# Performance work log

Measured on AMD Instinct MI355X. Metric: run time of the kernel, lower is better.

The kernel has to match this reference:

```python
import jax, jax.numpy as jnp
import numpy as np

CLUSTER_DIM = 64
SHRINKAGE = True
EPS = 1e-8


def setup_inputs() -> dict:
    key = jax.random.key(0)
    x = jax.random.normal(key, (256, CLUSTER_DIM, 4096), dtype=jnp.float32)
    return {"x": x}


def _mat_shrinkage(C, n):
    # Rao-Blackwellized Ledoit-Wolf shrinkage toward scaled identity.
    p = CLUSTER_DIM
    I = jnp.eye(p, dtype=C.dtype)[None, :, :]
    trace = jnp.trace(C, axis1=-2, axis2=-1)[:, None, None]          # [B,1,1]
    F_hat = trace / p * I
    second_trace = jnp.einsum('bij,bji->b', C, C)[:, None, None]      # tr(C @ C)
    numerator = (n - 2) / n * second_trace + trace ** 2
    denominator = (n + 2) * (second_trace - trace ** 2 / p)
    rho = jnp.minimum(numerator / denominator, 1.0)
    return rho * F_hat + (1.0 - rho) * C


def reference(x):
    B, C, M = x.shape  # C == CLUSTER_DIM
    x_mu = jnp.mean(x, axis=2, keepdims=True)
    x_cnt = x - x_mu                                                  # [B,C,M]
    cov = jnp.einsum('bcm,bdm->bcd', x_cnt, x_cnt) / M                # [B,C,C]
    if SHRINKAGE:
        cov = _mat_shrinkage(cov, n=M)
    L, Q = jnp.linalg.eigh(cov)                                       # L:[B,C] Q:[B,C,C]
    L = jnp.maximum(L, EPS)
    # S_hat = Q @ diag(L^-1/2) @ Q^T, fused as scaled columns of Q
    S_hat = jnp.einsum('bik,bk,bjk->bij', Q, jax.lax.rsqrt(L), Q)     # [B,C,C]
    Z = jnp.einsum('bij,bjm->bim', S_hat, x_cnt)                      # [B,C,M]
    return Z
```

## Files before the change

### kernel.cpp

```cpp
#include <hip/hip_runtime.h>
#include <hip/hip_bf16.h>

#define BB 256
#define P 64
#define MM 4096
#define MC 128
#define MT 256

using bf16x8 = __attribute__((ext_vector_type(8))) short;
using f32x16 = __attribute__((ext_vector_type(16))) float;
using f32x4  = __attribute__((ext_vector_type(4))) float;

__device__ inline f32x16 MF(bf16x8 a, bf16x8 b, f32x16 c) {
    return __builtin_amdgcn_mfma_f32_32x32x16_bf16(a, b, c, 0, 0, 0);
}
__device__ inline unsigned cvtpk(float lo, float hi) {
    unsigned u;
    asm("v_cvt_pk_bf16_f32 %0, %1, %2" : "=v"(u) : "v"(lo), "v"(hi));
    return u;
}

__global__ __launch_bounds__(256)
void covpart_kernel(const float* __restrict__ x, float* __restrict__ s2p,
                    float* __restrict__ s1p, int nsplit)
{
    __shared__ __align__(16) unsigned char smem[34816];

    const int b = blockIdx.x, sp = blockIdx.y;
    const int t = threadIdx.x;
    const int w = t >> 6, l = t & 63;
    const int lr = l & 31, lh = l >> 5;
    const int mlen = MM / nsplit;
    const float* xb = x + (size_t)b * (P * MM) + (size_t)sp * mlen;

    f32x16 acc0 = {0,0,0,0,0,0,0,0,0,0,0,0,0,0,0,0};
    f32x16 acc1 = {0,0,0,0,0,0,0,0,0,0,0,0,0,0,0,0};
    f32x16 acc2 = {0,0,0,0,0,0,0,0,0,0,0,0,0,0,0,0};
    float s1a[8] = {0.f,0.f,0.f,0.f,0.f,0.f,0.f,0.f};

    const int kbase = lh * 16;
    const int nch = mlen / MC;

    f32x4 v[8];
    #pragma unroll
    for (int j = 0; j < 8; ++j) {
        int f4 = t + 256 * j;
        int r = f4 >> 5, c = (f4 & 31) << 2;
        v[j] = *reinterpret_cast<const f32x4*>(xb + (size_t)r * MM + c);
    }

    for (int ch = 0; ch < nch; ++ch) {
        char* buf = (char*)smem + (ch & 1) * 17408;
        #pragma unroll
        for (int j = 0; j < 8; ++j) {
            int f4 = t + 256 * j;
            int r = f4 >> 5, c4 = f4 & 31;
            float e0 = v[j].x, e1 = v[j].y, e2 = v[j].z, e3 = v[j].w;
            s1a[j] += (e0 + e1) + (e2 + e3);
            uint2 hp;
            hp.x = cvtpk(e0, e1);
            hp.y = cvtpk(e2, e3);
            *reinterpret_cast<uint2*>(buf + r * 272 + c4 * 8) = hp;
        }
        if (ch + 1 < nch) {
            const int m0 = (ch + 1) * MC;
            #pragma unroll
            for (int j = 0; j < 8; ++j) {
                int f4 = t + 256 * j;
                int r = f4 >> 5, c = (f4 & 31) << 2;
                v[j] = *reinterpret_cast<const f32x4*>(xb + (size_t)r * MM + m0 + c);
            }
        }
        __syncthreads();
        #pragma unroll
        for (int kk = 0; kk < 2; ++kk) {
            const int kb = (2 * w + kk) * 32 + kbase;
            bf16x8 f0 = *(const bf16x8*)(buf + lr * 272 + kb);
            bf16x8 f1 = *(const bf16x8*)(buf + (32 + lr) * 272 + kb);
            acc0 = MF(f0, f0, acc0);
            acc1 = MF(f0, f1, acc1);
            acc2 = MF(f1, f1, acc2);
        }
    }

    float (*T)[32][33] = reinterpret_cast<float (*)[32][33]>(smem);
    float* s2b = s2p + ((size_t)sp * BB + b) * (P * P);

#define REDUCE_PASS(ACC, STORE)                                       \
    {                                                                 \
        __syncthreads();                                              \
        _Pragma("unroll")                                             \
        for (int n = 0; n < 16; ++n) {                                \
            int row = (n & 3) + 8 * (n >> 2) + 4 * lh;                \
            T[w][row][lr] = ACC[n];                                   \
        }                                                             \
        __syncthreads();                                              \
        _Pragma("unroll")                                             \
        for (int q = 0; q < 4; ++q) {                                 \
            int idx = t + 256 * q;                                    \
            int r = idx >> 5, c = idx & 31;                           \
            float s = T[0][r][c] + T[1][r][c] + T[2][r][c] + T[3][r][c]; \
            STORE                                                     \
        }                                                             \
    }

    REDUCE_PASS(acc0, s2b[r * 64 + c] = s;)
    REDUCE_PASS(acc1, s2b[r * 64 + 32 + c] = s; s2b[(32 + c) * 64 + r] = s;)
    REDUCE_PASS(acc2, s2b[(32 + r) * 64 + 32 + c] = s;)
#undef REDUCE_PASS

    #pragma unroll
    for (int m = 16; m >= 1; m >>= 1) {
        #pragma unroll
        for (int j = 0; j < 8; ++j) s1a[j] += __shfl_xor(s1a[j], m);
    }
    if ((l & 31) == 0) {
        float* s1b = s1p + ((size_t)sp * BB + b) * P;
        int r0 = 2 * w + lh;
        #pragma unroll
        for (int j = 0; j < 8; ++j) s1b[r0 + 8 * j] = s1a[j];
    }
}

typedef float (*Mat68)[68];

__device__ inline void mm64f(Mat68 D, Mat68 A, Mat68 Bm, int t, float alpha, float beta)
{
    __syncthreads();
    const int r0 = (t >> 4) * 4, c0 = (t & 15) * 4;
    float acc[4][4];
    #pragma unroll
    for (int i = 0; i < 4; ++i)
        #pragma unroll
        for (int j = 0; j < 4; ++j) acc[i][j] = 0.f;
    #pragma unroll 4
    for (int k = 0; k < P; ++k) {
        float av[4], bv[4];
        *reinterpret_cast<float4*>(av) = *reinterpret_cast<const float4*>(&A[k][r0]);
        *reinterpret_cast<float4*>(bv) = *reinterpret_cast<const float4*>(&Bm[k][c0]);
        #pragma unroll
        for (int i = 0; i < 4; ++i)
            #pragma unroll
            for (int j = 0; j < 4; ++j) acc[i][j] += av[i] * bv[j];
    }
    __syncthreads();
    #pragma unroll
    for (int i = 0; i < 4; ++i)
        #pragma unroll
        for (int j = 0; j < 4; ++j)
            D[r0 + i][c0 + j] = alpha * acc[i][j] + ((r0 + i) == (c0 + j) ? beta : 0.f);
}

__global__ __launch_bounds__(256)
void whiten_kernel(const float* __restrict__ s2p, const float* __restrict__ s1p,
                   unsigned* __restrict__ sbb, float* __restrict__ tvec, int nsplit)
{
    __shared__ __align__(16) float B0[P][68], B1[P][68], B2[P][68], B3[P][68], B4[P][68];
    __shared__ float mus[P];
    __shared__ float red[2][4];
    const int b = blockIdx.x, t = threadIdx.x;

    if (t < P) {
        float s = 0.f;
        for (int sp = 0; sp < nsplit; ++sp) s += s1p[((size_t)sp * BB + b) * P + t];
        mus[t] = s * (1.0f / MM);
    }
    __syncthreads();

    float tr_part = 0.f, s2_part = 0.f;
    #pragma unroll
    for (int j = 0; j < 16; ++j) {
        int f = t + 256 * j;
        int i = f >> 6, jc = f & 63;
        float sum = 0.f;
        for (int sp = 0; sp < nsplit; ++sp)
            sum += s2p[((size_t)sp * BB + b) * (P * P) + f];
        float v = sum * (1.0f / MM) - mus[i] * mus[jc];
        B0[i][jc] = v;
        s2_part += v * v;
        if (i == jc) tr_part += v;
    }
    #pragma unroll
    for (int off = 32; off > 0; off >>= 1) {
        tr_part += __shfl_down(tr_part, off);
        s2_part += __shfl_down(s2_part, off);
    }
    if ((t & 63) == 0) { red[0][t >> 6] = tr_part; red[1][t >> 6] = s2_part; }
    __syncthreads();
    const float trace = red[0][0] + red[0][1] + red[0][2] + red[0][3];
    const float sum2  = red[1][0] + red[1][1] + red[1][2] + red[1][3];

    const float nf = (float)MM;
    const float num = (nf - 2.0f) / nf * sum2 + trace * trace;
    const float den = (nf + 2.0f) * (sum2 - trace * trace / (float)P);
    const float rho = (den > 0.f) ? fminf(num / den, 1.0f) : 1.0f;
    const float lam = trace * (1.0f / P);
    const float inv_s = 1.0f / lam;

    #pragma unroll
    for (int j = 0; j < 16; ++j) {
        int f = t + 256 * j;
        int i = f >> 6, jc = f & 63;
        float v = B0[i][jc];
        float sv = ((1.0f - rho) * v + ((i == jc) ? rho * lam : 0.f)) * inv_s;
        B0[i][jc] = sv;
        B2[i][jc] = ((i == jc) ? 1.5f : 0.f) - 0.5f * sv;
    }

    mm64f(B1, B0, B2, t, 1.f, 0.f);
    Mat68 Yc = B1, Zc = B2, Tc = B0, U = B3, V = B4;
    {
        mm64f(Tc, Zc, Yc, t, -0.5f, 1.5f);
        mm64f(U,  Yc, Tc, t, 1.f, 0.f);
        mm64f(V,  Tc, Zc, t, 1.f, 0.f);
        Mat68 tmp = Yc; Yc = U; U = tmp;
        tmp = Zc; Zc = V; V = tmp;
    }
    mm64f(Tc, Zc, Yc, t, -0.5f, 1.5f);
    mm64f(U,  Tc, Zc, t, 1.f, 0.f);
    __syncthreads();

    const float sc = rsqrtf(lam);
    unsigned* sb = sbb + (size_t)b * (P * P / 2);
    #pragma unroll
    for (int j = 0; j < 8; ++j) {
        int slot = t + 256 * j;
        int dp = slot >> 6, row = slot & 63;
        sb[slot] = cvtpk(U[row][2 * dp] * sc, U[row][2 * dp + 1] * sc);
    }
    if (t < P) {
        float tv = 0.f;
        #pragma unroll
        for (int d = 0; d < P; ++d) tv += U[t][d] * mus[d];
        tvec[b * P + t] = tv * sc;
    }
}

__global__ __launch_bounds__(256)
void apply_kernel(const float* __restrict__ x, const unsigned* __restrict__ sbb,
                  const float* __restrict__ tvec, float* __restrict__ out)
{
    __shared__ unsigned Spk[32][68];
    __shared__ unsigned Xpk[32][260];
    __shared__ float tvs[P];
    const int mt = blockIdx.x, b = blockIdx.y;
    const int t = threadIdx.x;
    const int w = t >> 6, l = t & 63;
    const int lr = l & 31, lh = l >> 5;

    const unsigned* sb = sbb + (size_t)b * (P * P / 2);
    #pragma unroll
    for (int j = 0; j < 8; ++j) {
        int slot = t + 256 * j;
        Spk[slot >> 6][slot & 63] = sb[slot];
    }
    if (t < P) tvs[t] = tvec[b * P + t];

    const float* xb = x + (size_t)b * (P * MM) + mt * MT;
    #pragma unroll
    for (int j = 0; j < 8; ++j) {
        int slot = t + 256 * j;
        int dp = slot >> 6, m0 = (slot & 63) * 4;
        const float* xr = xb + (size_t)(2 * dp) * MM + m0;
        f32x4 a = __builtin_nontemporal_load(reinterpret_cast<const f32x4*>(xr));
        f32x4 c = __builtin_nontemporal_load(reinterpret_cast<const f32x4*>(xr + MM));
        uint4 pk = make_uint4(cvtpk(a.x, c.x), cvtpk(a.y, c.y),
                              cvtpk(a.z, c.z), cvtpk(a.w, c.w));
        *reinterpret_cast<uint4*>(&Xpk[dp][m0]) = pk;
    }
    __syncthreads();

    union U8 { unsigned u[4]; bf16x8 v; };
    bf16x8 sa0[4], sa1[4];
    #pragma unroll
    for (int ks = 0; ks < 4; ++ks) {
        const int dpb = ks * 8 + lh * 4;
        U8 x0, x1;
        #pragma unroll
        for (int q = 0; q < 4; ++q) {
            x0.u[q] = Spk[dpb + q][lr];
            x1.u[q] = Spk[dpb + q][32 + lr];
        }
        sa0[ks] = x0.v;
        sa1[ks] = x1.v;
    }

    f32x16 acc00 = {0,0,0,0,0,0,0,0,0,0,0,0,0,0,0,0};
    f32x16 acc01 = {0,0,0,0,0,0,0,0,0,0,0,0,0,0,0,0};
    f32x16 acc10 = {0,0,0,0,0,0,0,0,0,0,0,0,0,0,0,0};
    f32x16 acc11 = {0,0,0,0,0,0,0,0,0,0,0,0,0,0,0,0};

    const int cq0 = (2 * w) * 32 + lr, cq1 = cq0 + 32;
    #pragma unroll
    for (int ks = 0; ks < 4; ++ks) {
        const int dpb = ks * 8 + lh * 4;
        U8 b0, b1;
        #pragma unroll
        for (int q = 0; q < 4; ++q) {
            b0.u[q] = Xpk[dpb + q][cq0];
            b1.u[q] = Xpk[dpb + q][cq1];
        }
        acc00 = MF(sa0[ks], b0.v, acc00);
        acc01 = MF(sa0[ks], b1.v, acc01);
        acc10 = MF(sa1[ks], b0.v, acc10);
        acc11 = MF(sa1[ks], b1.v, acc11);
    }

    float* ob = out + (size_t)b * (P * MM) + mt * MT;
#define STORE_TILE(ACC, RT, CQ)                                          \
    {                                                                    \
        _Pragma("unroll")                                                \
        for (int n = 0; n < 16; ++n) {                                   \
            int row = (RT) * 32 + (n & 3) + 8 * (n >> 2) + 4 * lh;       \
            __builtin_nontemporal_store(ACC[n] - tvs[row],               \
                                        ob + (size_t)row * MM + (CQ));   \
        }                                                                \
    }
    STORE_TILE(acc00, 0, cq0)
    STORE_TILE(acc01, 0, cq1)
    STORE_TILE(acc10, 1, cq0)
    STORE_TILE(acc11, 1, cq1)
#undef STORE_TILE
}

extern "C" void kernel_launch(void* const* d_in, const int* in_sizes, int n_in,
                              void* d_out, int out_size, void* d_ws, size_t ws_size,
                              hipStream_t stream)
{
    const float* x = (const float*)d_in[0];
    float* out = (float*)d_out;

    auto need = [](int ns) -> size_t {
        return ((size_t)ns * BB * P * P + (size_t)ns * BB * P
                + (size_t)BB * P * P / 2 + (size_t)BB * P) * sizeof(float);
    };
    int nsplit = 4;
    if (ws_size < need(4)) nsplit = 2;
    if (ws_size < need(2)) nsplit = 1;

    float* s2p  = (float*)d_ws;
    float* s1p  = s2p + (size_t)nsplit * BB * P * P;
    unsigned* sbb = (unsigned*)(s1p + (size_t)nsplit * BB * P);
    float* tvec = (float*)(sbb + (size_t)BB * P * P / 2);

    covpart_kernel<<<dim3(BB, nsplit), 256, 0, stream>>>(x, s2p, s1p, nsplit);
    whiten_kernel<<<dim3(BB), 256, 0, stream>>>(s2p, s1p, sbb, tvec, nsplit);
    apply_kernel<<<dim3(MM / MT, BB), 256, 0, stream>>>(x, sbb, tvec, out);
}
```

Measured before the change: 196.2 us.

## Write packed bf16 copy of x in covariance pass and read it in apply

While computing covariance partials, the first kernel now also writes a row-pair-packed bf16 copy of x to workspace. The apply kernel reads that half-size buffer instead of re-reading fp32 x and converting it. This is meant to cut the apply kernel's read traffic. The price is an extra 64 MB of workspace writes in the first pass, and the path turns on only when the workspace is large enough. The fallback apply kernel also drops its nontemporal loads.

```diff
diff --git a/kernel.cpp b/kernel.cpp
--- a/kernel.cpp
+++ b/kernel.cpp
@@ -10,6 +10,8 @@
 using bf16x8 = __attribute__((ext_vector_type(8))) short;
 using f32x16 = __attribute__((ext_vector_type(16))) float;
 using f32x4  = __attribute__((ext_vector_type(4))) float;
+using u32x4  = __attribute__((ext_vector_type(4))) unsigned;
+using u32x2  = __attribute__((ext_vector_type(2))) unsigned;
 
 __device__ inline f32x16 MF(bf16x8 a, bf16x8 b, f32x16 c) {
     return __builtin_amdgcn_mfma_f32_32x32x16_bf16(a, b, c, 0, 0, 0);
@@ -20,9 +22,10 @@
     return u;
 }
 
+template<bool XPK>
 __global__ __launch_bounds__(256)
 void covpart_kernel(const float* __restrict__ x, float* __restrict__ s2p,
-                    float* __restrict__ s1p, int nsplit)
+                    float* __restrict__ s1p, unsigned* __restrict__ xpk, int nsplit)
 {
     __shared__ __align__(16) unsigned char smem[34816];
 
@@ -32,43 +35,59 @@
     const int lr = l & 31, lh = l >> 5;
     const int mlen = MM / nsplit;
     const float* xb = x + (size_t)b * (P * MM) + (size_t)sp * mlen;
+    unsigned* xpb = XPK ? (xpk + (size_t)b * (32 * MM) + (size_t)sp * mlen) : nullptr;
 
     f32x16 acc0 = {0,0,0,0,0,0,0,0,0,0,0,0,0,0,0,0};
     f32x16 acc1 = {0,0,0,0,0,0,0,0,0,0,0,0,0,0,0,0};
     f32x16 acc2 = {0,0,0,0,0,0,0,0,0,0,0,0,0,0,0,0};
-    float s1a[8] = {0.f,0.f,0.f,0.f,0.f,0.f,0.f,0.f};
+    float s1e[4] = {0.f,0.f,0.f,0.f};
+    float s1o[4] = {0.f,0.f,0.f,0.f};
 
     const int kbase = lh * 16;
     const int nch = mlen / MC;
 
-    f32x4 v[8];
-    #pragma unroll
-    for (int j = 0; j < 8; ++j) {
-        int f4 = t + 256 * j;
-        int r = f4 >> 5, c = (f4 & 31) << 2;
-        v[j] = *reinterpret_cast<const f32x4*>(xb + (size_t)r * MM + c);
+    f32x4 ve[4], vo[4];
+    #pragma unroll
+    for (int j = 0; j < 4; ++j) {
+        int slot = t + 256 * j;
+        int dp = slot >> 5, c = (slot & 31) << 2;
+        const float* p = xb + (size_t)(2 * dp) * MM + c;
+        ve[j] = *reinterpret_cast<const f32x4*>(p);
+        vo[j] = *reinterpret_cast<const f32x4*>(p + MM);
     }
 
     for (int ch = 0; ch < nch; ++ch) {
         char* buf = (char*)smem + (ch & 1) * 17408;
         #pragma unroll
-        for (int j = 0; j < 8; ++j) {
-            int f4 = t + 256 * j;
-            int r = f4 >> 5, c4 = f4 & 31;
-            float e0 = v[j].x, e1 = v[j].y, e2 = v[j].z, e3 = v[j].w;
-            s1a[j] += (e0 + e1) + (e2 + e3);
-            uint2 hp;
-            hp.x = cvtpk(e0, e1);
-            hp.y = cvtpk(e2, e3);
-            *reinterpret_cast<uint2*>(buf + r * 272 + c4 * 8) = hp;
+        for (int j = 0; j < 4; ++j) {
+            int slot = t + 256 * j;
+            int dp = slot >> 5, c4 = slot & 31;
+            float e0 = ve[j].x, e1 = ve[j].y, e2 = ve[j].z, e3 = ve[j].w;
+            float o0 = vo[j].x, o1 = vo[j].y, o2 = vo[j].z, o3 = vo[j].w;
+            s1e[j] += (e0 + e1) + (e2 + e3);
+            s1o[j] += (o0 + o1) + (o2 + o3);
+            u32x2 he, ho;
+            he.x = cvtpk(e0, e1); he.y = cvtpk(e2, e3);
+            ho.x = cvtpk(o0, o1); ho.y = cvtpk(o2, o3);
+            char* dst = buf + (2 * dp) * 272 + c4 * 8;
+            *reinterpret_cast<u32x2*>(dst) = he;
+            *reinterpret_cast<u32x2*>(dst + 272) = ho;
+            if (XPK) {
+                u32x4 pd;
+                pd.x = cvtpk(e0, o0); pd.y = cvtpk(e1, o1);
+                pd.z = cvtpk(e2, o2); pd.w = cvtpk(e3, o3);
+                *reinterpret_cast<u32x4*>(xpb + (size_t)dp * MM + ch * MC + c4 * 4) = pd;
+            }
         }
         if (ch + 1 < nch) {
             const int m0 = (ch + 1) * MC;
             #pragma unroll
-            for (int j = 0; j < 8; ++j) {
-                int f4 = t + 256 * j;
-                int r = f4 >> 5, c = (f4 & 31) << 2;
-                v[j] = *reinterpret_cast<const f32x4*>(xb + (size_t)r * MM + m0 + c);
+            for (int j = 0; j < 4; ++j) {
+                int slot = t + 256 * j;
+                int dp = slot >> 5, c = (slot & 31) << 2;
+                const float* p = xb + (size_t)(2 * dp) * MM + m0 + c;
+                ve[j] = *reinterpret_cast<const f32x4*>(p);
+                vo[j] = *reinterpret_cast<const f32x4*>(p + MM);
             }
         }
         __syncthreads();
@@ -112,13 +131,20 @@
     #pragma unroll
     for (int m = 16; m >= 1; m >>= 1) {
         #pragma unroll
-        for (int j = 0; j < 8; ++j) s1a[j] += __shfl_xor(s1a[j], m);
-    }
-    if ((l & 31) == 0) {
+        for (int j = 0; j < 4; ++j) {
+            s1e[j] += __shfl_xor(s1e[j], m);
+            s1o[j] += __shfl_xor(s1o[j], m);
+        }
+    }
+    if ((t & 31) == 0) {
         float* s1b = s1p + ((size_t)sp * BB + b) * P;
-        int r0 = 2 * w + lh;
-        #pragma unroll
-        for (int j = 0; j < 8; ++j) s1b[r0 + 8 * j] = s1a[j];
+        int g = t >> 5;
+        #pragma unroll
+        for (int j = 0; j < 4; ++j) {
+            int r0 = 2 * (g + 8 * j);
+            s1b[r0]     = s1e[j];
+            s1b[r0 + 1] = s1o[j];
+        }
     }
 }
 
@@ -237,8 +263,8 @@
 }
 
 __global__ __launch_bounds__(256)
-void apply_kernel(const float* __restrict__ x, const unsigned* __restrict__ sbb,
-                  const float* __restrict__ tvec, float* __restrict__ out)
+void apply_kernel_x(const unsigned* __restrict__ xpk, const unsigned* __restrict__ sbb,
+                    const float* __restrict__ tvec, float* __restrict__ out)
 {
     __shared__ unsigned Spk[32][68];
     __shared__ unsigned Xpk[32][260];
@@ -256,17 +282,13 @@
     }
     if (t < P) tvs[t] = tvec[b * P + t];
 
-    const float* xb = x + (size_t)b * (P * MM) + mt * MT;
+    const unsigned* xb = xpk + (size_t)b * (32 * MM) + mt * MT;
     #pragma unroll
     for (int j = 0; j < 8; ++j) {
         int slot = t + 256 * j;
         int dp = slot >> 6, m0 = (slot & 63) * 4;
-        const float* xr = xb + (size_t)(2 * dp) * MM + m0;
-        f32x4 a = __builtin_nontemporal_load(reinterpret_cast<const f32x4*>(xr));
-        f32x4 c = __builtin_nontemporal_load(reinterpret_cast<const f32x4*>(xr + MM));
-        uint4 pk = make_uint4(cvtpk(a.x, c.x), cvtpk(a.y, c.y),
-                              cvtpk(a.z, c.z), cvtpk(a.w, c.w));
-        *reinterpret_cast<uint4*>(&Xpk[dp][m0]) = pk;
+        u32x4 pk = *reinterpret_cast<const u32x4*>(xb + (size_t)dp * MM + m0);
+        *reinterpret_cast<u32x4*>(&Xpk[dp][m0]) = pk;
     }
     __syncthreads();
 
@@ -323,6 +345,93 @@
 #undef STORE_TILE
 }
 
+__global__ __launch_bounds__(256)
+void apply_kernel(const float* __restrict__ x, const unsigned* __restrict__ sbb,
+                  const float* __restrict__ tvec, float* __restrict__ out)
+{
+    __shared__ unsigned Spk[32][68];
+    __shared__ unsigned Xpk[32][260];
+    __shared__ float tvs[P];
+    const int mt = blockIdx.x, b = blockIdx.y;
+    const int t = threadIdx.x;
+    const int w = t >> 6, l = t & 63;
+    const int lr = l & 31, lh = l >> 5;
+
+    const unsigned* sb = sbb + (size_t)b * (P * P / 2);
+    #pragma unroll
+    for (int j = 0; j < 8; ++j) {
+        int slot = t + 256 * j;
+        Spk[slot >> 6][slot & 63] = sb[slot];
+    }
+    if (t < P) tvs[t] = tvec[b * P + t];
+
+    const float* xb = x + (size_t)b * (P * MM) + mt * MT;
+    #pragma unroll
+    for (int j = 0; j < 8; ++j) {
+        int slot = t + 256 * j;
+        int dp = slot >> 6, m0 = (slot & 63) * 4;
+        const float* xr = xb + (size_t)(2 * dp) * MM + m0;
+        f32x4 a = *reinterpret_cast<const f32x4*>(xr);
+        f32x4 c = *reinterpret_cast<const f32x4*>(xr + MM);
+        uint4 pk = make_uint4(cvtpk(a.x, c.x), cvtpk(a.y, c.y),
+                              cvtpk(a.z, c.z), cvtpk(a.w, c.w));
+        *reinterpret_cast<uint4*>(&Xpk[dp][m0]) = pk;
+    }
+    __syncthreads();
+
+    union U8 { unsigned u[4]; bf16x8 v; };
+    bf16x8 sa0[4], sa1[4];
+    #pragma unroll
+    for (int ks = 0; ks < 4; ++ks) {
+        const int dpb = ks * 8 + lh * 4;
+        U8 x0, x1;
+        #pragma unroll
+        for (int q = 0; q < 4; ++q) {
+            x0.u[q] = Spk[dpb + q][lr];
+            x1.u[q] = Spk[dpb + q][32 + lr];
+        }
+        sa0[ks] = x0.v;
+        sa1[ks] = x1.v;
+    }
+
+    f32x16 acc00 = {0,0,0,0,0,0,0,0,0,0,0,0,0,0,0,0};
+    f32x16 acc01 = {0,0,0,0,0,0,0,0,0,0,0,0,0,0,0,0};
+    f32x16 acc10 = {0,0,0,0,0,0,0,0,0,0,0,0,0,0,0,0};
+    f32x16 acc11 = {0,0,0,0,0,0,0,0,0,0,0,0,0,0,0,0};
+
+    const int cq0 = (2 * w) * 32 + lr, cq1 = cq0 + 32;
+    #pragma unroll
+    for (int ks = 0; ks < 4; ++ks) {
+        const int dpb = ks * 8 + lh * 4;
+        U8 b0, b1;
+        #pragma unroll
+        for (int q = 0; q < 4; ++q) {
+            b0.u[q] = Xpk[dpb + q][cq0];
+            b1.u[q] = Xpk[dpb + q][cq1];
+        }
+        acc00 = MF(sa0[ks], b0.v, acc00);
+        acc01 = MF(sa0[ks], b1.v, acc01);
+        acc10 = MF(sa1[ks], b0.v, acc10);
+        acc11 = MF(sa1[ks], b1.v, acc11);
+    }
+
+    float* ob = out + (size_t)b * (P * MM) + mt * MT;
+#define STORE_TILE(ACC, RT, CQ)                                          \
+    {                                                                    \
+        _Pragma("unroll")                                                \
+        for (int n = 0; n < 16; ++n) {                                   \
+            int row = (RT) * 32 + (n & 3) + 8 * (n >> 2) + 4 * lh;       \
+            __builtin_nontemporal_store(ACC[n] - tvs[row],               \
+                                        ob + (size_t)row * MM + (CQ));   \
+        }                                                                \
+    }
+    STORE_TILE(acc00, 0, cq0)
+    STORE_TILE(acc01, 0, cq1)
+    STORE_TILE(acc10, 1, cq0)
+    STORE_TILE(acc11, 1, cq1)
+#undef STORE_TILE
+}
+
 extern "C" void kernel_launch(void* const* d_in, const int* in_sizes, int n_in,
                               void* d_out, int out_size, void* d_ws, size_t ws_size,
                               hipStream_t stream)
@@ -334,16 +443,30 @@
         return ((size_t)ns * BB * P * P + (size_t)ns * BB * P
                 + (size_t)BB * P * P / 2 + (size_t)BB * P) * sizeof(float);
     };
-    int nsplit = 4;
-    if (ws_size < need(4)) nsplit = 2;
-    if (ws_size < need(2)) nsplit = 1;
+    const size_t xpk_bytes = (size_t)BB * 32 * MM * sizeof(unsigned);
+
+    int nsplit;
+    bool xon;
+    if (ws_size >= need(4) + xpk_bytes)      { nsplit = 4; xon = true; }
+    else if (ws_size >= need(2) + xpk_bytes) { nsplit = 2; xon = true; }
+    else {
+        xon = false;
+        nsplit = (ws_size >= need(4)) ? 4 : (ws_size >= need(2)) ? 2 : 1;
+    }
 
     float* s2p  = (float*)d_ws;
     float* s1p  = s2p + (size_t)nsplit * BB * P * P;
     unsigned* sbb = (unsigned*)(s1p + (size_t)nsplit * BB * P);
     float* tvec = (float*)(sbb + (size_t)BB * P * P / 2);
-
-    covpart_kernel<<<dim3(BB, nsplit), 256, 0, stream>>>(x, s2p, s1p, nsplit);
-    whiten_kernel<<<dim3(BB), 256, 0, stream>>>(s2p, s1p, sbb, tvec, nsplit);
-    apply_kernel<<<dim3(MM / MT, BB), 256, 0, stream>>>(x, sbb, tvec, out);
-}
+    unsigned* xpk = (unsigned*)(tvec + (size_t)BB * P);
+
+    if (xon) {
+        covpart_kernel<true><<<dim3(BB, nsplit), 256, 0, stream>>>(x, s2p, s1p, xpk, nsplit);
+        whiten_kernel<<<dim3(BB), 256, 0, stream>>>(s2p, s1p, sbb, tvec, nsplit);
+        apply_kernel_x<<<dim3(MM / MT, BB), 256, 0, stream>>>(xpk, sbb, tvec, out);
+    } else {
+        covpart_kernel<false><<<dim3(BB, nsplit), 256, 0, stream>>>(x, s2p, s1p, nullptr, nsplit);
+        whiten_kernel<<<dim3(BB), 256, 0, stream>>>(s2p, s1p, sbb, tvec, nsplit);
+        apply_kernel<<<dim3(MM / MT, BB), 256, 0, stream>>>(x, sbb, tvec, out);
+    }
+}
```

After: 187.0 us. 1.05x faster.

## Fuse covariance and whitening kernels and stage packed bf16 x for apply

Applied to the files above, without the earlier changes.

Merges the split covariance kernel and the whitening kernel into one 1024-thread block per batch. Each block accumulates the full covariance with MFMA, builds the centered covariance in LDS, and runs the Newton-Schulz iterations on 256 of its threads. This drops the partial-sum workspace round trip and one launch. The same kernel also writes a bf16 pair-packed copy of x, so the apply kernel reads half the bytes instead of re-reading fp32 x and converting it. The cost is a large extra write and a large new workspace buffer with no size check. It also uses fewer, larger blocks with a serial whitening tail during which most threads sit idle.

```diff
diff --git a/kernel.cpp b/kernel.cpp
--- a/kernel.cpp
+++ b/kernel.cpp
@@ -4,12 +4,15 @@
 #define BB 256
 #define P 64
 #define MM 4096
-#define MC 128
+#define MC2 512
+#define RS 1040
 #define MT 256
 
 using bf16x8 = __attribute__((ext_vector_type(8))) short;
 using f32x16 = __attribute__((ext_vector_type(16))) float;
 using f32x4  = __attribute__((ext_vector_type(4))) float;
+using u32x4  = __attribute__((ext_vector_type(4))) unsigned;
+using u32x2  = __attribute__((ext_vector_type(2))) unsigned;
 
 __device__ inline f32x16 MF(bf16x8 a, bf16x8 b, f32x16 c) {
     return __builtin_amdgcn_mfma_f32_32x32x16_bf16(a, b, c, 0, 0, 0);
@@ -20,73 +23,145 @@
     return u;
 }
 
-__global__ __launch_bounds__(256)
-void covpart_kernel(const float* __restrict__ x, float* __restrict__ s2p,
-                    float* __restrict__ s1p, int nsplit)
+typedef float (*M68)[68];
+
+__device__ inline void mmg(M68 D, M68 A, M68 Bm, int t, float alpha, float beta)
 {
-    __shared__ __align__(16) unsigned char smem[34816];
-
-    const int b = blockIdx.x, sp = blockIdx.y;
+    __syncthreads();
+    float acc[4][4];
+    const int r0 = (t >> 4) * 4, c0 = (t & 15) * 4;
+    if (t < 256) {
+        #pragma unroll
+        for (int i = 0; i < 4; ++i)
+            #pragma unroll
+            for (int j = 0; j < 4; ++j) acc[i][j] = 0.f;
+        #pragma unroll 4
+        for (int k = 0; k < P; ++k) {
+            float av[4], bv[4];
+            *reinterpret_cast<float4*>(av) = *reinterpret_cast<const float4*>(&A[k][r0]);
+            *reinterpret_cast<float4*>(bv) = *reinterpret_cast<const float4*>(&Bm[k][c0]);
+            #pragma unroll
+            for (int i = 0; i < 4; ++i)
+                #pragma unroll
+                for (int j = 0; j < 4; ++j) acc[i][j] += av[i] * bv[j];
+        }
+    }
+    __syncthreads();
+    if (t < 256) {
+        #pragma unroll
+        for (int i = 0; i < 4; ++i)
+            #pragma unroll
+            for (int j = 0; j < 4; ++j)
+                D[r0 + i][c0 + j] = alpha * acc[i][j] + ((r0 + i) == (c0 + j) ? beta : 0.f);
+    }
+}
+
+__global__ __launch_bounds__(1024)
+void covwhiten_kernel(const float* __restrict__ x, unsigned* __restrict__ xpk,
+                      unsigned* __restrict__ sbb, float* __restrict__ tvec)
+{
+    __shared__ __align__(16) unsigned char smem[133120];
+    __shared__ float mus[P];
+    __shared__ float red[2][16];
+    __shared__ float s1red[16][4][2];
+
+    const int b = blockIdx.x;
     const int t = threadIdx.x;
     const int w = t >> 6, l = t & 63;
     const int lr = l & 31, lh = l >> 5;
-    const int mlen = MM / nsplit;
-    const float* xb = x + (size_t)b * (P * MM) + (size_t)sp * mlen;
+    const float* xb = x + (size_t)b * (P * MM);
+    unsigned* xpb = xpk + (size_t)b * (32 * MM);
 
     f32x16 acc0 = {0,0,0,0,0,0,0,0,0,0,0,0,0,0,0,0};
     f32x16 acc1 = {0,0,0,0,0,0,0,0,0,0,0,0,0,0,0,0};
     f32x16 acc2 = {0,0,0,0,0,0,0,0,0,0,0,0,0,0,0,0};
-    float s1a[8] = {0.f,0.f,0.f,0.f,0.f,0.f,0.f,0.f};
-
+    float s1e[4] = {0.f,0.f,0.f,0.f};
+    float s1o[4] = {0.f,0.f,0.f,0.f};
     const int kbase = lh * 16;
-    const int nch = mlen / MC;
-
-    f32x4 v[8];
-    #pragma unroll
-    for (int j = 0; j < 8; ++j) {
-        int f4 = t + 256 * j;
-        int r = f4 >> 5, c = (f4 & 31) << 2;
-        v[j] = *reinterpret_cast<const f32x4*>(xb + (size_t)r * MM + c);
-    }
-
-    for (int ch = 0; ch < nch; ++ch) {
-        char* buf = (char*)smem + (ch & 1) * 17408;
-        #pragma unroll
-        for (int j = 0; j < 8; ++j) {
-            int f4 = t + 256 * j;
-            int r = f4 >> 5, c4 = f4 & 31;
-            float e0 = v[j].x, e1 = v[j].y, e2 = v[j].z, e3 = v[j].w;
-            s1a[j] += (e0 + e1) + (e2 + e3);
-            uint2 hp;
-            hp.x = cvtpk(e0, e1);
-            hp.y = cvtpk(e2, e3);
-            *reinterpret_cast<uint2*>(buf + r * 272 + c4 * 8) = hp;
-        }
-        if (ch + 1 < nch) {
-            const int m0 = (ch + 1) * MC;
+
+    f32x4 ve[4], vo[4];
+    #pragma unroll
+    for (int j = 0; j < 4; ++j) {
+        int slot = t + 1024 * j;
+        int dp = slot >> 7, c = (slot & 127) << 2;
+        const float* p = xb + (size_t)(2 * dp) * MM + c;
+        ve[j] = *reinterpret_cast<const f32x4*>(p);
+        vo[j] = *reinterpret_cast<const f32x4*>(p + MM);
+    }
+
+    for (int ch = 0; ch < MM / MC2; ++ch) {
+        char* buf = (char*)smem + (ch & 1) * 66560;
+        #pragma unroll
+        for (int j = 0; j < 4; ++j) {
+            int slot = t + 1024 * j;
+            int dp = slot >> 7, c4 = slot & 127;
+            float e0 = ve[j].x, e1 = ve[j].y, e2 = ve[j].z, e3 = ve[j].w;
+            float o0 = vo[j].x, o1 = vo[j].y, o2 = vo[j].z, o3 = vo[j].w;
+            s1e[j] += (e0 + e1) + (e2 + e3);
+            s1o[j] += (o0 + o1) + (o2 + o3);
+            u32x2 he, ho;
+            he.x = cvtpk(e0, e1); he.y = cvtpk(e2, e3);
+            ho.x = cvtpk(o0, o1); ho.y = cvtpk(o2, o3);
+            char* dst = buf + (2 * dp) * RS + c4 * 8;
+            *reinterpret_cast<u32x2*>(dst) = he;
+            *reinterpret_cast<u32x2*>(dst + RS) = ho;
+            u32x4 pd;
+            pd.x = cvtpk(e0, o0); pd.y = cvtpk(e1, o1);
+            pd.z = cvtpk(e2, o2); pd.w = cvtpk(e3, o3);
+            *reinterpret_cast<u32x4*>(xpb + (size_t)dp * MM + ch * MC2 + c4 * 4) = pd;
+        }
+        if (ch + 1 < MM / MC2) {
+            const int m0 = (ch + 1) * MC2;
             #pragma unroll
-            for (int j = 0; j < 8; ++j) {
-                int f4 = t + 256 * j;
-                int r = f4 >> 5, c = (f4 & 31) << 2;
-                v[j] = *reinterpret_cast<const f32x4*>(xb + (size_t)r * MM + m0 + c);
+            for (int j = 0; j < 4; ++j) {
+                int slot = t + 1024 * j;
+                int dp = slot >> 7, c = (slot & 127) << 2;
+                const float* p = xb + (size_t)(2 * dp) * MM + m0 + c;
+                ve[j] = *reinterpret_cast<const f32x4*>(p);
+                vo[j] = *reinterpret_cast<const f32x4*>(p + MM);
             }
         }
         __syncthreads();
         #pragma unroll
         for (int kk = 0; kk < 2; ++kk) {
             const int kb = (2 * w + kk) * 32 + kbase;
-            bf16x8 f0 = *(const bf16x8*)(buf + lr * 272 + kb);
-            bf16x8 f1 = *(const bf16x8*)(buf + (32 + lr) * 272 + kb);
+            bf16x8 f0 = *(const bf16x8*)(buf + lr * RS + kb);
+            bf16x8 f1 = *(const bf16x8*)(buf + (32 + lr) * RS + kb);
             acc0 = MF(f0, f0, acc0);
             acc1 = MF(f0, f1, acc1);
             acc2 = MF(f1, f1, acc2);
         }
     }
 
+    #pragma unroll
+    for (int m = 32; m >= 1; m >>= 1) {
+        #pragma unroll
+        for (int j = 0; j < 4; ++j) {
+            s1e[j] += __shfl_xor(s1e[j], m);
+            s1o[j] += __shfl_xor(s1o[j], m);
+        }
+    }
+    if (l == 0) {
+        #pragma unroll
+        for (int j = 0; j < 4; ++j) {
+            s1red[w][j][0] = s1e[j];
+            s1red[w][j][1] = s1o[j];
+        }
+    }
+    __syncthreads();
+    if (t < P) {
+        int par = t & 1, dh = t >> 1;
+        int d0 = dh & 7, jj = dh >> 3;
+        mus[t] = (s1red[2 * d0][jj][par] + s1red[2 * d0 + 1][jj][par]) * (1.0f / MM);
+    }
+
     float (*T)[32][33] = reinterpret_cast<float (*)[32][33]>(smem);
-    float* s2b = s2p + ((size_t)sp * BB + b) * (P * P);
-
-#define REDUCE_PASS(ACC, STORE)                                       \
+    M68 CM = reinterpret_cast<M68>((char*)smem + 69632);
+    const float invM = 1.0f / MM;
+    const int rr = t >> 5, cc = t & 31;
+    float trp = 0.f, s2p = 0.f;
+
+#define CREDUCE(ACC, BODY)                                            \
     {                                                                 \
         __syncthreads();                                              \
         _Pragma("unroll")                                             \
@@ -95,100 +170,38 @@
             T[w][row][lr] = ACC[n];                                   \
         }                                                             \
         __syncthreads();                                              \
-        _Pragma("unroll")                                             \
-        for (int q = 0; q < 4; ++q) {                                 \
-            int idx = t + 256 * q;                                    \
-            int r = idx >> 5, c = idx & 31;                           \
-            float s = T[0][r][c] + T[1][r][c] + T[2][r][c] + T[3][r][c]; \
-            STORE                                                     \
+        {                                                             \
+            float s = 0.f;                                            \
+            _Pragma("unroll")                                         \
+            for (int wv = 0; wv < 16; ++wv) s += T[wv][rr][cc];       \
+            BODY                                                      \
         }                                                             \
     }
 
-    REDUCE_PASS(acc0, s2b[r * 64 + c] = s;)
-    REDUCE_PASS(acc1, s2b[r * 64 + 32 + c] = s; s2b[(32 + c) * 64 + r] = s;)
-    REDUCE_PASS(acc2, s2b[(32 + r) * 64 + 32 + c] = s;)
-#undef REDUCE_PASS
-
-    #pragma unroll
-    for (int m = 16; m >= 1; m >>= 1) {
-        #pragma unroll
-        for (int j = 0; j < 8; ++j) s1a[j] += __shfl_xor(s1a[j], m);
-    }
-    if ((l & 31) == 0) {
-        float* s1b = s1p + ((size_t)sp * BB + b) * P;
-        int r0 = 2 * w + lh;
-        #pragma unroll
-        for (int j = 0; j < 8; ++j) s1b[r0 + 8 * j] = s1a[j];
-    }
-}
-
-typedef float (*Mat68)[68];
-
-__device__ inline void mm64f(Mat68 D, Mat68 A, Mat68 Bm, int t, float alpha, float beta)
-{
-    __syncthreads();
-    const int r0 = (t >> 4) * 4, c0 = (t & 15) * 4;
-    float acc[4][4];
-    #pragma unroll
-    for (int i = 0; i < 4; ++i)
-        #pragma unroll
-        for (int j = 0; j < 4; ++j) acc[i][j] = 0.f;
-    #pragma unroll 4
-    for (int k = 0; k < P; ++k) {
-        float av[4], bv[4];
-        *reinterpret_cast<float4*>(av) = *reinterpret_cast<const float4*>(&A[k][r0]);
-        *reinterpret_cast<float4*>(bv) = *reinterpret_cast<const float4*>(&Bm[k][c0]);
-        #pragma unroll
-        for (int i = 0; i < 4; ++i)
-            #pragma unroll
-            for (int j = 0; j < 4; ++j) acc[i][j] += av[i] * bv[j];
-    }
-    __syncthreads();
-    #pragma unroll
-    for (int i = 0; i < 4; ++i)
-        #pragma unroll
-        for (int j = 0; j < 4; ++j)
-            D[r0 + i][c0 + j] = alpha * acc[i][j] + ((r0 + i) == (c0 + j) ? beta : 0.f);
-}
-
-__global__ __launch_bounds__(256)
-void whiten_kernel(const float* __restrict__ s2p, const float* __restrict__ s1p,
-                   unsigned* __restrict__ sbb, float* __restrict__ tvec, int nsplit)
-{
-    __shared__ __align__(16) float B0[P][68], B1[P][68], B2[P][68], B3[P][68], B4[P][68];
-    __shared__ float mus[P];
-    __shared__ float red[2][4];
-    const int b = blockIdx.x, t = threadIdx.x;
-
-    if (t < P) {
-        float s = 0.f;
-        for (int sp = 0; sp < nsplit; ++sp) s += s1p[((size_t)sp * BB + b) * P + t];
-        mus[t] = s * (1.0f / MM);
-    }
-    __syncthreads();
-
-    float tr_part = 0.f, s2_part = 0.f;
-    #pragma unroll
-    for (int j = 0; j < 16; ++j) {
-        int f = t + 256 * j;
-        int i = f >> 6, jc = f & 63;
-        float sum = 0.f;
-        for (int sp = 0; sp < nsplit; ++sp)
-            sum += s2p[((size_t)sp * BB + b) * (P * P) + f];
-        float v = sum * (1.0f / MM) - mus[i] * mus[jc];
-        B0[i][jc] = v;
-        s2_part += v * v;
-        if (i == jc) tr_part += v;
-    }
-    #pragma unroll
-    for (int off = 32; off > 0; off >>= 1) {
-        tr_part += __shfl_down(tr_part, off);
-        s2_part += __shfl_down(s2_part, off);
-    }
-    if ((t & 63) == 0) { red[0][t >> 6] = tr_part; red[1][t >> 6] = s2_part; }
-    __syncthreads();
-    const float trace = red[0][0] + red[0][1] + red[0][2] + red[0][3];
-    const float sum2  = red[1][0] + red[1][1] + red[1][2] + red[1][3];
+    CREDUCE(acc0, {
+        float v = s * invM - mus[rr] * mus[cc];
+        CM[rr][cc] = v; s2p += v * v; if (rr == cc) trp += v;
+    })
+    CREDUCE(acc1, {
+        float v = s * invM - mus[rr] * mus[32 + cc];
+        CM[rr][32 + cc] = v; CM[32 + cc][rr] = v; s2p += 2.f * v * v;
+    })
+    CREDUCE(acc2, {
+        float v = s * invM - mus[32 + rr] * mus[32 + cc];
+        CM[32 + rr][32 + cc] = v; s2p += v * v; if (rr == cc) trp += v;
+    })
+#undef CREDUCE
+
+    #pragma unroll
+    for (int m = 32; m >= 1; m >>= 1) {
+        trp += __shfl_xor(trp, m);
+        s2p += __shfl_xor(s2p, m);
+    }
+    if (l == 0) { red[0][w] = trp; red[1][w] = s2p; }
+    __syncthreads();
+    float trace = 0.f, sum2 = 0.f;
+    #pragma unroll
+    for (int wv = 0; wv < 16; ++wv) { trace += red[0][wv]; sum2 += red[1][wv]; }
 
     const float nf = (float)MM;
     const float num = (nf - 2.0f) / nf * sum2 + trace * trace;
@@ -197,48 +210,46 @@
     const float lam = trace * (1.0f / P);
     const float inv_s = 1.0f / lam;
 
-    #pragma unroll
-    for (int j = 0; j < 16; ++j) {
-        int f = t + 256 * j;
+    M68 M1 = reinterpret_cast<M68>(smem);
+    M68 M2 = reinterpret_cast<M68>((char*)smem + 17408);
+    M68 M3 = reinterpret_cast<M68>((char*)smem + 34816);
+    #pragma unroll
+    for (int jj = 0; jj < 4; ++jj) {
+        int f = t + 1024 * jj;
         int i = f >> 6, jc = f & 63;
-        float v = B0[i][jc];
+        float v = CM[i][jc];
         float sv = ((1.0f - rho) * v + ((i == jc) ? rho * lam : 0.f)) * inv_s;
-        B0[i][jc] = sv;
-        B2[i][jc] = ((i == jc) ? 1.5f : 0.f) - 0.5f * sv;
-    }
-
-    mm64f(B1, B0, B2, t, 1.f, 0.f);
-    Mat68 Yc = B1, Zc = B2, Tc = B0, U = B3, V = B4;
-    {
-        mm64f(Tc, Zc, Yc, t, -0.5f, 1.5f);
-        mm64f(U,  Yc, Tc, t, 1.f, 0.f);
-        mm64f(V,  Tc, Zc, t, 1.f, 0.f);
-        Mat68 tmp = Yc; Yc = U; U = tmp;
-        tmp = Zc; Zc = V; V = tmp;
-    }
-    mm64f(Tc, Zc, Yc, t, -0.5f, 1.5f);
-    mm64f(U,  Tc, Zc, t, 1.f, 0.f);
+        CM[i][jc] = sv;
+        M2[i][jc] = ((i == jc) ? 1.5f : 0.f) - 0.5f * sv;
+    }
+
+    mmg(M1, CM, M2, t, 1.f, 0.f);
+    mmg(CM, M2, M1, t, -0.5f, 1.5f);
+    mmg(M3, M1, CM, t, 1.f, 0.f);
+    mmg(M1, CM, M2, t, 1.f, 0.f);
+    mmg(M2, M1, M3, t, -0.5f, 1.5f);
+    mmg(M3, M2, M1, t, 1.f, 0.f);
     __syncthreads();
 
     const float sc = rsqrtf(lam);
     unsigned* sb = sbb + (size_t)b * (P * P / 2);
     #pragma unroll
-    for (int j = 0; j < 8; ++j) {
-        int slot = t + 256 * j;
+    for (int j = 0; j < 2; ++j) {
+        int slot = t + 1024 * j;
         int dp = slot >> 6, row = slot & 63;
-        sb[slot] = cvtpk(U[row][2 * dp] * sc, U[row][2 * dp + 1] * sc);
+        sb[slot] = cvtpk(M3[row][2 * dp] * sc, M3[row][2 * dp + 1] * sc);
     }
     if (t < P) {
         float tv = 0.f;
         #pragma unroll
-        for (int d = 0; d < P; ++d) tv += U[t][d] * mus[d];
+        for (int d = 0; d < P; ++d) tv += M3[t][d] * mus[d];
         tvec[b * P + t] = tv * sc;
     }
 }
 
 __global__ __launch_bounds__(256)
-void apply_kernel(const float* __restrict__ x, const unsigned* __restrict__ sbb,
-                  const float* __restrict__ tvec, float* __restrict__ out)
+void apply_kernel_x(const unsigned* __restrict__ xpk, const unsigned* __restrict__ sbb,
+                    const float* __restrict__ tvec, float* __restrict__ out)
 {
     __shared__ unsigned Spk[32][68];
     __shared__ unsigned Xpk[32][260];
@@ -256,17 +267,13 @@
     }
     if (t < P) tvs[t] = tvec[b * P + t];
 
-    const float* xb = x + (size_t)b * (P * MM) + mt * MT;
+    const unsigned* xb = xpk + (size_t)b * (32 * MM) + mt * MT;
     #pragma unroll
     for (int j = 0; j < 8; ++j) {
         int slot = t + 256 * j;
         int dp = slot >> 6, m0 = (slot & 63) * 4;
-        const float* xr = xb + (size_t)(2 * dp) * MM + m0;
-        f32x4 a = __builtin_nontemporal_load(reinterpret_cast<const f32x4*>(xr));
-        f32x4 c = __builtin_nontemporal_load(reinterpret_cast<const f32x4*>(xr + MM));
-        uint4 pk = make_uint4(cvtpk(a.x, c.x), cvtpk(a.y, c.y),
-                              cvtpk(a.z, c.z), cvtpk(a.w, c.w));
-        *reinterpret_cast<uint4*>(&Xpk[dp][m0]) = pk;
+        u32x4 pk = *reinterpret_cast<const u32x4*>(xb + (size_t)dp * MM + m0);
+        *reinterpret_cast<u32x4*>(&Xpk[dp][m0]) = pk;
     }
     __syncthreads();
 
@@ -330,20 +337,10 @@
     const float* x = (const float*)d_in[0];
     float* out = (float*)d_out;
 
-    auto need = [](int ns) -> size_t {
-        return ((size_t)ns * BB * P * P + (size_t)ns * BB * P
-                + (size_t)BB * P * P / 2 + (size_t)BB * P) * sizeof(float);
-    };
-    int nsplit = 4;
-    if (ws_size < need(4)) nsplit = 2;
-    if (ws_size < need(2)) nsplit = 1;
-
-    float* s2p  = (float*)d_ws;
-    float* s1p  = s2p + (size_t)nsplit * BB * P * P;
-    unsigned* sbb = (unsigned*)(s1p + (size_t)nsplit * BB * P);
+    unsigned* sbb = (unsigned*)d_ws;
     float* tvec = (float*)(sbb + (size_t)BB * P * P / 2);
-
-    covpart_kernel<<<dim3(BB, nsplit), 256, 0, stream>>>(x, s2p, s1p, nsplit);
-    whiten_kernel<<<dim3(BB), 256, 0, stream>>>(s2p, s1p, sbb, tvec, nsplit);
-    apply_kernel<<<dim3(MM / MT, BB), 256, 0, stream>>>(x, sbb, tvec, out);
-}
+    unsigned* xpk = (unsigned*)(tvec + (size_t)BB * P);
+
+    covwhiten_kernel<<<dim3(BB), 1024, 0, stream>>>(x, xpk, sbb, tvec);
+    apply_kernel_x<<<dim3(MM / MT, BB), 256, 0, stream>>>(xpk, sbb, tvec, out);
+}
```

New measurement: 223.2 us. 1.14x slower.
